# Performance work log

Measured on AMD Instinct MI355X. Metric: run time of the kernel, lower is better.

Reference implementation:

```python
import jax, jax.numpy as jnp
import numpy as np

D_IN = 1024
D_OUT = 1024
N_HEADS = 16
HEAD_DIM = D_OUT // N_HEADS


def setup_inputs() -> dict:
    key = jax.random.key(0)
    ks = jax.random.split(key, 6)
    s = 0.02
    return {
        "x": jax.random.normal(ks[0], (2, 2048, D_IN), dtype=jnp.float32),
        "W_q": jax.random.normal(ks[1], (D_IN, D_OUT), dtype=jnp.float32) * s,
        "W_k": jax.random.normal(ks[2], (D_IN, D_OUT), dtype=jnp.float32) * s,
        "W_v": jax.random.normal(ks[3], (D_IN, D_OUT), dtype=jnp.float32) * s,
        "W_o": jax.random.normal(ks[4], (D_OUT, D_OUT), dtype=jnp.float32) * s,
        "b_o": jax.random.normal(ks[5], (D_OUT,), dtype=jnp.float32) * s,
    }


def reference(x, W_q, W_k, W_v, W_o, b_o):
    b, n, _ = x.shape
    # project and split heads: [b, h, n, d]
    q = (x @ W_q).reshape(b, n, N_HEADS, HEAD_DIM).transpose(0, 2, 1, 3)
    k = (x @ W_k).reshape(b, n, N_HEADS, HEAD_DIM).transpose(0, 2, 1, 3)
    v = (x @ W_v).reshape(b, n, N_HEADS, HEAD_DIM).transpose(0, 2, 1, 3)
    scores = jnp.einsum("bhqd,bhkd->bhqk", q, k)
    # causal mask: positions k > q masked with -inf (applied BEFORE scaling, as in source)
    causal = jnp.tril(jnp.ones((n, n), dtype=bool))
    scores = jnp.where(causal, scores, -jnp.inf)
    scale = HEAD_DIM ** 0.5
    attn = jax.nn.softmax(scores / scale, axis=-1)
    ctx = jnp.einsum("bhqk,bhkd->bhqd", attn, v)
    ctx = ctx.transpose(0, 2, 1, 3).reshape(b, n, D_OUT)
    return ctx @ W_o + b_o
```

## Files before the change

kernel.cpp:

```cpp
#include <hip/hip_runtime.h>
#include <hip/hip_bf16.h>


typedef __bf16 bf16x8 __attribute__((ext_vector_type(8)));
typedef __bf16 bf16x4 __attribute__((ext_vector_type(4)));
typedef float  f32x4  __attribute__((ext_vector_type(4)));

typedef __attribute__((address_space(1))) void gas_void;
typedef __attribute__((address_space(3))) void las_void;

__device__ __forceinline__ void gload_lds16(const void* g, void* l) {
  __builtin_amdgcn_global_load_lds((gas_void*)g, (las_void*)l, 16, 0, 0);
}

#define FULL_DRAIN() asm volatile("s_waitcnt vmcnt(0) lgkmcnt(0)" ::: "memory")
#define SCHED_FENCE() __builtin_amdgcn_sched_barrier(0)

#define QSCALE 0.18033688011112042f

__global__ void cvt_f32_bf16_k(const float* __restrict__ in, __bf16* __restrict__ out, int n4) {
  int i = blockIdx.x * 256 + threadIdx.x;
  if (i >= n4) return;
  float4 v = ((const float4*)in)[i];
  bf16x4 o = { (__bf16)v.x, (__bf16)v.y, (__bf16)v.z, (__bf16)v.w };
  ((bf16x4*)out)[i] = o;
}

__global__ void transpose_w4_k(const float* __restrict__ Wq, const float* __restrict__ Wk,
                               const float* __restrict__ Wv, const float* __restrict__ Wo,
                               __bf16* __restrict__ wtqkv, __bf16* __restrict__ wot) {
  __shared__ float tile[32][33];
  const int z = blockIdx.z;
  const float* in = z == 0 ? Wq : z == 1 ? Wk : z == 2 ? Wv : Wo;
  __bf16* out = z < 3 ? wtqkv + (size_t)z * 1048576 : wot;
  const int bx = blockIdx.x, by = blockIdx.y;
  const int tx = threadIdx.x, ty = threadIdx.y;
#pragma unroll
  for (int i = 0; i < 4; ++i)
    tile[ty + i * 8][tx] = in[(by * 32 + ty + i * 8) * 1024 + bx * 32 + tx];
  __syncthreads();
#pragma unroll
  for (int i = 0; i < 4; ++i)
    out[(size_t)(bx * 32 + ty + i * 8) * 1024 + by * 32 + tx] = (__bf16)tile[tx][ty + i * 8];
}

__device__ __forceinline__ bf16x8 lds_swz32(const __bf16* base, int row, int cb) {
  const char* p = (const char*)base + row * 64 + (cb ^ (((row >> 1) & 3) << 4));
  return *(const bf16x8*)p;
}

template<int MODE>
__global__ __launch_bounds__(256) void gemm_bt_k(
    const __bf16* __restrict__ A, const __bf16* __restrict__ Bt,
    __bf16* __restrict__ qo, __bf16* __restrict__ ko, __bf16* __restrict__ vo,
    float* __restrict__ outf, const float* __restrict__ bias)
{
  __shared__ __align__(16) __bf16 As[3][4096];
  __shared__ __align__(16) __bf16 Bs[3][4096];

  const int t = threadIdx.x;
  const int l = t & 63;
  const int w = t >> 6;
  const int wr = w >> 1, wc = w & 1;
  const int lr = l & 15;
  const int lkb = (l >> 4) * 16;
  const int bm = blockIdx.x, bn = blockIdx.y;

  const int swz_el = ((t & 3) * 8) ^ (((t >> 3) & 3) << 3);
  const __bf16* a0 = A + (size_t)(bm * 128 + (t >> 2)) * 1024 + swz_el;
  const __bf16* b0 = Bt + (size_t)(bn * 128 + (t >> 2)) * 1024 + swz_el;

  f32x4 acc[4][4] = {};

#define STAGE(kt_, buf_)                                          \
  do {                                                            \
    const int k0_ = (kt_) * 32;                                   \
    gload_lds16(a0 + k0_, As[buf_] + t * 8);                      \
    gload_lds16(a0 + 64 * 1024 + k0_, As[buf_] + 2048 + t * 8);   \
    gload_lds16(b0 + k0_, Bs[buf_] + t * 8);                      \
    gload_lds16(b0 + 64 * 1024 + k0_, Bs[buf_] + 2048 + t * 8);   \
  } while (0)

  STAGE(0, 0);
  STAGE(1, 1);
  SCHED_FENCE();
  asm volatile("s_waitcnt vmcnt(4)" ::: "memory");
  __builtin_amdgcn_s_barrier();
  SCHED_FENCE();

  int bc = 0, bs = 2;
  for (int kt = 0; kt < 32; ++kt) {
    if (kt < 30) STAGE(kt + 2, bs);
    SCHED_FENCE();

    bf16x8 af[4], bfr[4];
#pragma unroll
    for (int m = 0; m < 4; ++m)
      af[m] = lds_swz32(As[bc], wr * 64 + m * 16 + lr, lkb);
#pragma unroll
    for (int n = 0; n < 4; ++n)
      bfr[n] = lds_swz32(Bs[bc], wc * 64 + n * 16 + lr, lkb);
#pragma unroll
    for (int m = 0; m < 4; ++m)
#pragma unroll
      for (int n = 0; n < 4; ++n)
        acc[m][n] = __builtin_amdgcn_mfma_f32_16x16x32_bf16(af[m], bfr[n], acc[m][n], 0, 0, 0);

    SCHED_FENCE();
    if (kt < 30) asm volatile("s_waitcnt vmcnt(4)" ::: "memory");
    else         asm volatile("s_waitcnt vmcnt(0)" ::: "memory");
    __builtin_amdgcn_s_barrier();
    SCHED_FENCE();
    bc = (bc == 2) ? 0 : bc + 1;
    bs = (bs == 2) ? 0 : bs + 1;
  }
#undef STAGE

#pragma unroll
  for (int m = 0; m < 4; ++m) {
    const int rg = bm * 128 + wr * 64 + m * 16 + (l >> 4) * 4;
#pragma unroll
    for (int n = 0; n < 4; ++n) {
      const int cg = bn * 128 + wc * 64 + n * 16 + lr;
      if (MODE == 0) {
        const int proj = cg >> 10, within = cg & 1023;
        const int h = within >> 6, d = within & 63;
#pragma unroll
        for (int r = 0; r < 4; ++r) {
          const int row = rg + r;
          const int b = row >> 11, pos = row & 2047;
          const int bh = b * 16 + h;
          if (proj == 0) {
            qo[((size_t)bh * 2048 + pos) * 64 + d] = (__bf16)(acc[m][n][r] * QSCALE);
          } else if (proj == 1) {
            const int tile = pos >> 6, rr = pos & 63;
            const int off = rr * 128 + ((d * 2) ^ ((rr & 7) << 4));
            *(__bf16*)((char*)ko + ((size_t)bh * 32 + tile) * 8192 + off) = (__bf16)acc[m][n][r];
          } else {
            const int tile = pos >> 6, cc = pos & 63;
            const int off = d * 128 + ((cc * 2) ^ ((d & 7) << 4));
            *(__bf16*)((char*)vo + ((size_t)bh * 32 + tile) * 8192 + off) = (__bf16)acc[m][n][r];
          }
        }
      } else {
#pragma unroll
        for (int r = 0; r < 4; ++r)
          outf[(size_t)(rg + r) * 1024 + cg] = acc[m][n][r] + bias[cg];
      }
    }
  }
}

__device__ __forceinline__ bf16x8 lds_swz(const __bf16* base, int row, int cb) {
  const char* p = (const char*)base + row * 128 + (cb ^ ((row & 7) << 4));
  return *(const bf16x8*)p;
}

__global__ __launch_bounds__(512) void attn_fwd_k(
    const __bf16* __restrict__ Q, const __bf16* __restrict__ K,
    const __bf16* __restrict__ V, __bf16* __restrict__ ctx)
{
  __shared__ __align__(16) char smem[53760];
  __bf16* Kbuf = (__bf16*)smem;
  __bf16* Vbuf = (__bf16*)(smem + 16384);
  __bf16* PsB  = (__bf16*)(smem + 32768);
  float*  LsX  = (float*)(smem + 53248);
  float*  xch  = (float*)smem;

  const int n = blockIdx.x;
  const int bh = (n & 255) >> 3;
  const int pp = n & 7;
  const int qt = (n >> 8) ? pp : 15 - pp;
  const int nkt = 2 * qt + 2;

  const int t = threadIdx.x, l = t & 63, w = t >> 6;
  const int lr = l & 15, lg = l >> 4;
  const int qb = w & 3;
  const int kvh = w >> 2;

  const __bf16* qptr = Q + (size_t)bh * 131072;
  const __bf16* kptr = K + (size_t)bh * 131072;
  const __bf16* vptr = V + (size_t)bh * 131072;
  __bf16* Ps = PsB + w * 1280;

  bf16x8 qf[2][2];
#pragma unroll
  for (int m = 0; m < 2; ++m)
#pragma unroll
    for (int h2 = 0; h2 < 2; ++h2)
      qf[m][h2] = *(const bf16x8*)(qptr + (size_t)(qt * 128 + qb * 32 + m * 16 + lr) * 64 + h2 * 32 + lg * 8);

  f32x4 o[2][4] = {};
  f32x4 lsum[2] = {};

  gload_lds16(kptr + t * 8, Kbuf + t * 8);
  gload_lds16(vptr + t * 8, Vbuf + t * 8);
  FULL_DRAIN();
  __syncthreads();
  SCHED_FENCE();

  for (int kt = 0; kt < nkt; ++kt) {
    const int cur = kt & 1;
    if (kt + 1 < nkt) {
      gload_lds16(kptr + (kt + 1) * 4096 + t * 8, Kbuf + (cur ^ 1) * 4096 + t * 8);
      gload_lds16(vptr + (kt + 1) * 4096 + t * 8, Vbuf + (cur ^ 1) * 4096 + t * 8);
    }
    SCHED_FENCE();
    const __bf16* Kb = Kbuf + cur * 4096;
    const __bf16* Vb = Vbuf + cur * 4096;

    bf16x8 kf[2][2];
#pragma unroll
    for (int ng = 0; ng < 2; ++ng)
#pragma unroll
      for (int h2 = 0; h2 < 2; ++h2)
        kf[ng][h2] = lds_swz(Kb, kvh * 32 + ng * 16 + lr, h2 * 64 + lg * 16);

    f32x4 s[2][2];
#pragma unroll
    for (int m = 0; m < 2; ++m)
#pragma unroll
      for (int ng = 0; ng < 2; ++ng) {
        f32x4 z = {};
        z = __builtin_amdgcn_mfma_f32_16x16x32_bf16(qf[m][0], kf[ng][0], z, 0, 0, 0);
        s[m][ng] = __builtin_amdgcn_mfma_f32_16x16x32_bf16(qf[m][1], kf[ng][1], z, 0, 0, 0);
      }

    if (kt >= 2 * qt) {
#pragma unroll
      for (int m = 0; m < 2; ++m) {
        const int qpos = qt * 128 + qb * 32 + m * 16 + lg * 4;
#pragma unroll
        for (int ng = 0; ng < 2; ++ng) {
          const int kv = kt * 64 + kvh * 32 + ng * 16 + lr;
#pragma unroll
          for (int r = 0; r < 4; ++r)
            if (kv > qpos + r) s[m][ng][r] = -1e30f;
        }
      }
    }

#pragma unroll
    for (int m = 0; m < 2; ++m)
#pragma unroll
      for (int ng = 0; ng < 2; ++ng)
#pragma unroll
        for (int r = 0; r < 4; ++r) {
          const float p = __builtin_amdgcn_exp2f(s[m][ng][r]);
          lsum[m][r] += p;
          Ps[(m * 16 + lg * 4 + r) * 40 + ng * 16 + lr] = (__bf16)p;
        }

    asm volatile("s_waitcnt lgkmcnt(0)" ::: "memory");
    SCHED_FENCE();

    bf16x8 pf[2];
#pragma unroll
    for (int m = 0; m < 2; ++m)
      pf[m] = *(const bf16x8*)(Ps + (m * 16 + lr) * 40 + lg * 8);
    bf16x8 vf[4];
#pragma unroll
    for (int ngd = 0; ngd < 4; ++ngd)
      vf[ngd] = lds_swz(Vb, ngd * 16 + lr, kvh * 64 + lg * 16);
#pragma unroll
    for (int m = 0; m < 2; ++m)
#pragma unroll
      for (int ngd = 0; ngd < 4; ++ngd)
        o[m][ngd] = __builtin_amdgcn_mfma_f32_16x16x32_bf16(pf[m], vf[ngd], o[m][ngd], 0, 0, 0);

    FULL_DRAIN();
    __syncthreads();
    SCHED_FENCE();
  }

#pragma unroll
  for (int m = 0; m < 2; ++m)
#pragma unroll
    for (int r = 0; r < 4; ++r) {
      float v = lsum[m][r];
      v += __shfl_xor(v, 1);
      v += __shfl_xor(v, 2);
      v += __shfl_xor(v, 4);
      v += __shfl_xor(v, 8);
      lsum[m][r] = v;
    }

  if (kvh == 1) {
#pragma unroll
    for (int m = 0; m < 2; ++m)
#pragma unroll
      for (int ngd = 0; ngd < 4; ++ngd)
#pragma unroll
        for (int r = 0; r < 4; ++r)
          xch[qb * 2048 + (m * 16 + lg * 4 + r) * 64 + ngd * 16 + lr] = o[m][ngd][r];
    if (lr == 0) {
#pragma unroll
      for (int m = 0; m < 2; ++m)
#pragma unroll
        for (int r = 0; r < 4; ++r)
          LsX[qb * 32 + m * 16 + lg * 4 + r] = lsum[m][r];
    }
  }
  FULL_DRAIN();
  __syncthreads();
  SCHED_FENCE();

  if (kvh == 0) {
    const int b_ = bh >> 4, h = bh & 15;
#pragma unroll
    for (int m = 0; m < 2; ++m)
#pragma unroll
      for (int r = 0; r < 4; ++r) {
        const float sum = lsum[m][r] + LsX[qb * 32 + m * 16 + lg * 4 + r];
        const float inv = 1.0f / sum;
        const int pos = qt * 128 + qb * 32 + m * 16 + lg * 4 + r;
#pragma unroll
        for (int ngd = 0; ngd < 4; ++ngd) {
          const float val = o[m][ngd][r] +
              xch[qb * 2048 + (m * 16 + lg * 4 + r) * 64 + ngd * 16 + lr];
          ctx[((size_t)(b_ * 2048 + pos)) * 1024 + h * 64 + ngd * 16 + lr] =
              (__bf16)(val * inv);
        }
      }
  }
}

extern "C" void kernel_launch(void* const* d_in, const int* in_sizes, int n_in,
                              void* d_out, int out_size, void* d_ws, size_t ws_size,
                              hipStream_t stream) {
  const float* x  = (const float*)d_in[0];
  const float* Wq = (const float*)d_in[1];
  const float* Wk = (const float*)d_in[2];
  const float* Wv = (const float*)d_in[3];
  const float* Wo = (const float*)d_in[4];
  const float* bo = (const float*)d_in[5];
  float* out = (float*)d_out;

  char* ws = (char*)d_ws;
  __bf16* xb    = (__bf16*)(ws);
  __bf16* wtqkv = (__bf16*)(ws + (8u << 20));
  __bf16* wot   = (__bf16*)(ws + (14u << 20));
  __bf16* qbuf  = (__bf16*)(ws + (16u << 20));
  __bf16* kbuf  = (__bf16*)(ws + (24u << 20));
  __bf16* vbuf  = (__bf16*)(ws + (32u << 20));
  __bf16* ctx   = (__bf16*)(ws + (40u << 20));

  cvt_f32_bf16_k<<<4096, 256, 0, stream>>>(x, xb, 1048576);
  transpose_w4_k<<<dim3(32, 32, 4), dim3(32, 8), 0, stream>>>(Wq, Wk, Wv, Wo, wtqkv, wot);

  gemm_bt_k<0><<<dim3(32, 24), 256, 0, stream>>>(xb, wtqkv, qbuf, kbuf, vbuf, nullptr, nullptr);
  attn_fwd_k<<<512, 512, 0, stream>>>(qbuf, kbuf, vbuf, ctx);
  gemm_bt_k<1><<<dim3(32, 8), 256, 0, stream>>>(ctx, wot, nullptr, nullptr, nullptr, out, bo);
}
```

Baseline: 106.6 us.

## Use 256x256 tile, 512-thread GEMM for fused QKV projection

Replaces the 128x128 QKV projection GEMM with a new 256x256-tile kernel using 8 waves, double-buffered BK=64 LDS stages loaded via global_load_lds, XOR-swizzled fragment reads, and setprio around MFMA bursts. The larger tile raises arithmetic intensity per LDS/global load, but the grid shrinks to 192 blocks on a 256-CU device, leaving some CUs idle, and extra intra-iteration barriers are added. The output projection GEMM is split out as a non-templated kernel with unchanged logic.

After: 122.6 us. +15.0%, slower.

```diff
diff --git a/kernel.cpp b/kernel.cpp
--- a/kernel.cpp
+++ b/kernel.cpp
@@ -44,15 +44,133 @@
     out[(size_t)(bx * 32 + ty + i * 8) * 1024 + by * 32 + tx] = (__bf16)tile[tx][ty + i * 8];
 }
 
+__device__ __forceinline__ bf16x8 rdfrag(const __bf16* base, int row, int kh, int lg, int lr) {
+  const int byte = (kh * 64 + lg * 16) ^ ((lr & 7) << 4);
+  return *(const bf16x8*)((const char*)base + row * 128 + byte);
+}
+
+__global__ __launch_bounds__(512) void gemm256_qkv_k(
+    const __bf16* __restrict__ A, const __bf16* __restrict__ Bt,
+    __bf16* __restrict__ qo, __bf16* __restrict__ ko, __bf16* __restrict__ vo)
+{
+  __shared__ __align__(16) __bf16 Abuf[2][256 * 64];
+  __shared__ __align__(16) __bf16 Bbuf[2][256 * 64];
+
+  const int t = threadIdx.x;
+  const int l = t & 63, w = t >> 6;
+  const int wm = w >> 2, wn = w & 3;
+  const int lr = l & 15, lg = l >> 4;
+  const int bm = blockIdx.x, bn = blockIdx.y;
+
+  const int swz_el = ((t & 7) * 8) ^ (((t >> 3) & 7) << 3);
+  const __bf16* aSrc = A  + (size_t)(bm * 256 + (t >> 3)) * 1024 + swz_el;
+  const __bf16* bSrc = Bt + (size_t)(bn * 256 + (t >> 3)) * 1024 + swz_el;
+
+  f32x4 acc[8][4] = {};
+
+#define STAGE8(buf_, kt_)                                                      \
+  do {                                                                         \
+    const int k0_ = (kt_) * 64;                                                \
+    _Pragma("unroll")                                                          \
+    for (int c_ = 0; c_ < 4; ++c_) {                                           \
+      gload_lds16(aSrc + (size_t)c_ * 65536 + k0_, Abuf[buf_] + c_ * 4096 + t * 8); \
+      gload_lds16(bSrc + (size_t)c_ * 65536 + k0_, Bbuf[buf_] + c_ * 4096 + t * 8); \
+    }                                                                          \
+  } while (0)
+
+  STAGE8(0, 0);
+  FULL_DRAIN();
+  __builtin_amdgcn_s_barrier();
+  SCHED_FENCE();
+
+  int cb = 0;
+  for (int kt = 0; kt < 16; ++kt) {
+    const __bf16* Ab = Abuf[cb];
+    const __bf16* Bb = Bbuf[cb];
+
+    if (kt < 15) STAGE8(cb ^ 1, kt + 1);
+    SCHED_FENCE();
+
+    bf16x8 bfr[4][2];
+#pragma unroll
+    for (int nf = 0; nf < 4; ++nf)
+#pragma unroll
+      for (int kh = 0; kh < 2; ++kh)
+        bfr[nf][kh] = rdfrag(Bb, wn * 64 + nf * 16 + lr, kh, lg, lr);
+
+#pragma unroll
+    for (int p = 0; p < 4; ++p) {
+      bf16x8 af[2][2];
+#pragma unroll
+      for (int i = 0; i < 2; ++i)
+#pragma unroll
+        for (int kh = 0; kh < 2; ++kh)
+          af[i][kh] = rdfrag(Ab, wm * 128 + (p * 2 + i) * 16 + lr, kh, lg, lr);
+
+      asm volatile("s_waitcnt lgkmcnt(0)" ::: "memory");
+      SCHED_FENCE();
+      __builtin_amdgcn_s_setprio(1);
+#pragma unroll
+      for (int i = 0; i < 2; ++i)
+#pragma unroll
+        for (int nf = 0; nf < 4; ++nf) {
+          acc[p * 2 + i][nf] = __builtin_amdgcn_mfma_f32_16x16x32_bf16(
+              af[i][0], bfr[nf][0], acc[p * 2 + i][nf], 0, 0, 0);
+          acc[p * 2 + i][nf] = __builtin_amdgcn_mfma_f32_16x16x32_bf16(
+              af[i][1], bfr[nf][1], acc[p * 2 + i][nf], 0, 0, 0);
+        }
+      __builtin_amdgcn_s_setprio(0);
+      SCHED_FENCE();
+      if (p < 3) {
+        __builtin_amdgcn_s_barrier();
+        SCHED_FENCE();
+      }
+    }
+
+    asm volatile("s_waitcnt vmcnt(0)" ::: "memory");
+    __builtin_amdgcn_s_barrier();
+    SCHED_FENCE();
+    cb ^= 1;
+  }
+#undef STAGE8
+
+#pragma unroll
+  for (int mf = 0; mf < 8; ++mf) {
+    const int rg = bm * 256 + wm * 128 + mf * 16 + lg * 4;
+#pragma unroll
+    for (int nf = 0; nf < 4; ++nf) {
+      const int cg = bn * 256 + wn * 64 + nf * 16 + lr;
+      const int proj = cg >> 10, within = cg & 1023;
+      const int h = within >> 6, d = within & 63;
+#pragma unroll
+      for (int r = 0; r < 4; ++r) {
+        const int row = rg + r;
+        const int b = row >> 11, pos = row & 2047;
+        const int bh = b * 16 + h;
+        const float v = acc[mf][nf][r];
+        if (proj == 0) {
+          qo[((size_t)bh * 2048 + pos) * 64 + d] = (__bf16)(v * QSCALE);
+        } else if (proj == 1) {
+          const int tile = pos >> 6, rr = pos & 63;
+          const int off = rr * 128 + ((d * 2) ^ ((rr & 7) << 4));
+          *(__bf16*)((char*)ko + ((size_t)bh * 32 + tile) * 8192 + off) = (__bf16)v;
+        } else {
+          const int tile = pos >> 6, cc = pos & 63;
+          const int off = d * 128 + ((cc * 2) ^ ((d & 7) << 4));
+          *(__bf16*)((char*)vo + ((size_t)bh * 32 + tile) * 8192 + off) = (__bf16)v;
+        }
+      }
+    }
+  }
+}
+
 __device__ __forceinline__ bf16x8 lds_swz32(const __bf16* base, int row, int cb) {
   const char* p = (const char*)base + row * 64 + (cb ^ (((row >> 1) & 3) << 4));
   return *(const bf16x8*)p;
 }
 
-template<int MODE>
-__global__ __launch_bounds__(256) void gemm_bt_k(
+__global__ __launch_bounds__(256) void gemm_out_k(
     const __bf16* __restrict__ A, const __bf16* __restrict__ Bt,
-    __bf16* __restrict__ qo, __bf16* __restrict__ ko, __bf16* __restrict__ vo,
     float* __restrict__ outf, const float* __restrict__ bias)
 {
   __shared__ __align__(16) __bf16 As[3][4096];
@@ -122,31 +240,9 @@
 #pragma unroll
     for (int n = 0; n < 4; ++n) {
       const int cg = bn * 128 + wc * 64 + n * 16 + lr;
-      if (MODE == 0) {
-        const int proj = cg >> 10, within = cg & 1023;
-        const int h = within >> 6, d = within & 63;
-#pragma unroll
-        for (int r = 0; r < 4; ++r) {
-          const int row = rg + r;
-          const int b = row >> 11, pos = row & 2047;
-          const int bh = b * 16 + h;
-          if (proj == 0) {
-            qo[((size_t)bh * 2048 + pos) * 64 + d] = (__bf16)(acc[m][n][r] * QSCALE);
-          } else if (proj == 1) {
-            const int tile = pos >> 6, rr = pos & 63;
-            const int off = rr * 128 + ((d * 2) ^ ((rr & 7) << 4));
-            *(__bf16*)((char*)ko + ((size_t)bh * 32 + tile) * 8192 + off) = (__bf16)acc[m][n][r];
-          } else {
-            const int tile = pos >> 6, cc = pos & 63;
-            const int off = d * 128 + ((cc * 2) ^ ((d & 7) << 4));
-            *(__bf16*)((char*)vo + ((size_t)bh * 32 + tile) * 8192 + off) = (__bf16)acc[m][n][r];
-          }
-        }
-      } else {
-#pragma unroll
-        for (int r = 0; r < 4; ++r)
-          outf[(size_t)(rg + r) * 1024 + cg] = acc[m][n][r] + bias[cg];
-      }
+#pragma unroll
+      for (int r = 0; r < 4; ++r)
+        outf[(size_t)(rg + r) * 1024 + cg] = acc[m][n][r] + bias[cg];
     }
   }
 }
@@ -348,7 +444,7 @@
   cvt_f32_bf16_k<<<4096, 256, 0, stream>>>(x, xb, 1048576);
   transpose_w4_k<<<dim3(32, 32, 4), dim3(32, 8), 0, stream>>>(Wq, Wk, Wv, Wo, wtqkv, wot);
 
-  gemm_bt_k<0><<<dim3(32, 24), 256, 0, stream>>>(xb, wtqkv, qbuf, kbuf, vbuf, nullptr, nullptr);
+  gemm256_qkv_k<<<dim3(16, 12), 512, 0, stream>>>(xb, wtqkv, qbuf, kbuf, vbuf);
   attn_fwd_k<<<512, 512, 0, stream>>>(qbuf, kbuf, vbuf, ctx);
-  gemm_bt_k<1><<<dim3(32, 8), 256, 0, stream>>>(ctx, wot, nullptr, nullptr, nullptr, out, bo);
-}
+  gemm_out_k<<<dim3(32, 8), 256, 0, stream>>>(ctx, wot, out, bo);
+}
```
